# Optimization experiments

Hardware: AMD Instinct MI355X
Metric: run time of the kernel (lower is better)

The kernel has to match this reference:

```python
import jax, jax.numpy as jnp
import numpy as np

WIN = 9
WIN_SIZE = float(WIN ** 3)
LBD = 1.0
EPS = 1e-5


def _box_sum(x, win=WIN):
    """Separable sum over a win^3 window with zero padding == conv3d with all-ones kernel."""
    pad = win // 2
    for ax in (2, 3, 4):  # spatial axes of [N, C, H, W, D]
        wd = [1] * 5
        wd[ax] = win
        padc = [(0, 0)] * 5
        padc[ax] = (pad, pad)
        x = jax.lax.reduce_window(x, 0.0, jax.lax.add, tuple(wd), (1, 1, 1, 1, 1), padc)
    return x


def _warp3d(images, flows):
    """Trilinear warp. images [B,G,C,H,W,D], flows [B,G,3,H,W,D] (voxel displacements,
    channels ordered as (H, W, D) axes). Border-clamped sampling."""
    B, G, C, H, W, D = images.shape
    N = B * G
    img = images.reshape(N, C, H, W, D)
    flo = flows.reshape(N, 3, H, W, D)
    ft = flo.dtype
    gh = jnp.arange(H, dtype=ft).reshape(H, 1, 1)
    gw = jnp.arange(W, dtype=ft).reshape(1, W, 1)
    gd = jnp.arange(D, dtype=ft).reshape(1, 1, D)
    ch = jnp.clip(flo[:, 0] + gh, 0.0, H - 1.0)
    cw = jnp.clip(flo[:, 1] + gw, 0.0, W - 1.0)
    cd = jnp.clip(flo[:, 2] + gd, 0.0, D - 1.0)
    h0f = jnp.floor(ch); w0f = jnp.floor(cw); d0f = jnp.floor(cd)
    fh = ch - h0f; fw = cw - w0f; fd = cd - d0f
    h0 = h0f.astype(jnp.int32); w0 = w0f.astype(jnp.int32); d0 = d0f.astype(jnp.int32)
    h1 = jnp.minimum(h0 + 1, H - 1)
    w1 = jnp.minimum(w0 + 1, W - 1)
    d1 = jnp.minimum(d0 + 1, D - 1)
    flat = img.reshape(N, C, H * W * D)

    def gather(hi, wi, di):
        lin = ((hi * W + wi) * D + di).reshape(N, 1, H * W * D)
        return jnp.take_along_axis(flat, lin, axis=2).reshape(N, C, H, W, D)

    out = jnp.zeros_like(img)
    for hi, wh in ((h0, 1.0 - fh), (h1, fh)):
        for wi, ww in ((w0, 1.0 - fw), (w1, fw)):
            for di, wdw in ((d0, 1.0 - fd), (d1, fd)):
                w8 = (wh * ww * wdw)[:, None]  # [N,1,H,W,D]
                out = out + w8 * gather(hi, wi, di)
    return out.reshape(B, G, C, H, W, D)


def setup_inputs() -> dict:
    key = jax.random.key(0)
    k1, k2 = jax.random.split(key)
    images = jax.random.normal(k1, (1, 4, 1, 128, 128, 128), dtype=jnp.float32)
    warps = jax.random.normal(k2, (1, 4, 3, 128, 128, 128), dtype=jnp.float32)
    return {"images": images, "warps": warps}


def reference(images, warps):
    B, G, C, H, W, D = images.shape
    warped = _warp3d(images, warps).reshape(B * G, C, H, W, D)
    # groupwise template = mean over the B*G warped volumes, broadcast back
    template = jnp.broadcast_to(jnp.mean(warped, axis=0, keepdims=True), warped.shape)
    Ii, Ji = template, warped
    # 5 stat channels: I, J, I^2, J^2, IJ; groups=5 box-filter conv == per-channel box sum
    stats = jnp.concatenate([Ii, Ji, Ii * Ii, Ji * Ji, Ii * Ji], axis=1)
    sums = _box_sum(stats)
    I_sum, J_sum, I2_sum, J2_sum, IJ_sum = jnp.split(sums, 5, axis=1)
    cross = IJ_sum - J_sum / WIN_SIZE * I_sum
    I_var = I2_sum - I_sum / WIN_SIZE * I_sum
    J_var = J2_sum - J_sum / WIN_SIZE * J_sum
    cc = cross * cross / (I_var * J_var + EPS)
    lncc = -jnp.mean(cc)
    # Grad3d('l2') on warps [B,G,3,H,W,D]: dx over H (axis 3), dy over W (axis 4), dz over D (axis 5)
    dx = jnp.square(warps[:, :, :, 1:] - warps[:, :, :, :-1])
    dy = jnp.square(warps[:, :, :, :, 1:] - warps[:, :, :, :, :-1])
    dz = jnp.square(warps[..., 1:] - warps[..., :-1])
    g2 = (jnp.mean(dx) + jnp.mean(dy) + jnp.mean(dz)) / 3.0
    return lncc + LBD * g2
```

## Files before the change

### kernel.cpp

```cpp
#include <hip/hip_runtime.h>
#include <hip/hip_bf16.h>


#define NVOX (128*128*128)
#define NGRP 4
#define NCH 14

__global__ __launch_bounds__(256) void k_warp_stats_d(
    const float* __restrict__ img, const float* __restrict__ flo,
    float* __restrict__ S, double* __restrict__ pg2, int blk0)
{
    __shared__ float jt[NGRP][256];
    int t = threadIdx.x;
    int b = blk0 + ((blockIdx.x & 7) << 8) + (blockIdx.x >> 3);
    int v = b * 256 + t;
    int d = v & 127;
    int w = (v >> 7) & 127;
    int h = v >> 14;
    float g2s = 0.f;

#pragma unroll
    for (int g = 0; g < NGRP; ++g) {
        const float* f = flo + (size_t)g * 3 * NVOX;
        float fx = f[v], fy = f[NVOX + v], fz = f[2 * NVOX + v];
        if (h < 127) {
            float a = f[v + 16384] - fx;
            float bb = f[NVOX + v + 16384] - fy;
            float c = f[2 * NVOX + v + 16384] - fz;
            g2s += a * a + bb * bb + c * c;
        }
        if (w < 127) {
            float a = f[v + 128] - fx;
            float bb = f[NVOX + v + 128] - fy;
            float c = f[2 * NVOX + v + 128] - fz;
            g2s += a * a + bb * bb + c * c;
        }
        if (d < 127) {
            float a = f[v + 1] - fx;
            float bb = f[NVOX + v + 1] - fy;
            float c = f[2 * NVOX + v + 1] - fz;
            g2s += a * a + bb * bb + c * c;
        }
        float ch = fminf(fmaxf(fx + (float)h, 0.f), 127.f);
        float cw = fminf(fmaxf(fy + (float)w, 0.f), 127.f);
        float cd = fminf(fmaxf(fz + (float)d, 0.f), 127.f);
        float h0f = floorf(ch), w0f = floorf(cw), d0f = floorf(cd);
        int h0 = (int)h0f, w0 = (int)w0f, d0 = (int)d0f;
        float fh = ch - h0f, fw = cw - w0f, fd = cd - d0f;
        int h1 = min(h0 + 1, 127), w1 = min(w0 + 1, 127), d1 = min(d0 + 1, 127);
        const float* im = img + (size_t)g * NVOX;
        int b00 = (h0 * 128 + w0) * 128;
        int b01 = (h0 * 128 + w1) * 128;
        int b10 = (h1 * 128 + w0) * 128;
        int b11 = (h1 * 128 + w1) * 128;
        float v000 = im[b00 + d0], v001 = im[b00 + d1];
        float v010 = im[b01 + d0], v011 = im[b01 + d1];
        float v100 = im[b10 + d0], v101 = im[b10 + d1];
        float v110 = im[b11 + d0], v111 = im[b11 + d1];
        float c00 = v000 + fd * (v001 - v000);
        float c01 = v010 + fd * (v011 - v010);
        float c10 = v100 + fd * (v101 - v100);
        float c11 = v110 + fd * (v111 - v110);
        float c0 = c00 + fw * (c01 - c00);
        float c1 = c10 + fw * (c11 - c10);
        jt[g][t] = c0 + fh * (c1 - c0);
    }
    __syncthreads();

    float s[NCH];
#pragma unroll
    for (int c = 0; c < NCH; ++c) s[c] = 0.f;
    int lbase = t & 128;
#pragma unroll
    for (int k = -4; k <= 4; ++k) {
        int q = d + k;
        if ((unsigned)q < 128u) {
            int tq = lbase + q;
            float j0 = jt[0][tq], j1 = jt[1][tq], j2 = jt[2][tq], j3 = jt[3][tq];
            float tm = 0.25f * (j0 + j1 + j2 + j3);
            s[0] += tm;       s[1] += tm * tm;
            s[2] += j0;  s[3] += j0 * j0;  s[4]  += tm * j0;
            s[5] += j1;  s[6] += j1 * j1;  s[7]  += tm * j1;
            s[8] += j2;  s[9] += j2 * j2;  s[10] += tm * j2;
            s[11] += j3; s[12] += j3 * j3; s[13] += tm * j3;
        }
    }
#pragma unroll
    for (int c = 0; c < NCH; ++c) S[(size_t)c * NVOX + v] = s[c];

    double val = (double)g2s;
    for (int off = 32; off; off >>= 1) val += __shfl_down(val, off, 64);
    __shared__ double wsum[4];
    int lane = t & 63, wid = t >> 6;
    if (lane == 0) wsum[wid] = val;
    __syncthreads();
    if (t == 0) pg2[b] = wsum[0] + wsum[1] + wsum[2] + wsum[3];
}

__global__ __launch_bounds__(256) void k_sum_w(float* __restrict__ S)
{
    __shared__ float tile[128 * 68];
    int t = threadIdx.x;
    int bid = blockIdx.x;
    int half = bid & 1;
    int chh = bid >> 1;
    size_t base = (size_t)chh * 16384 + half * 64;
#pragma unroll
    for (int it = 0; it < 8; ++it) {
        int idx4 = it * 256 + t;
        int w = idx4 >> 4, dq = idx4 & 15;
        *(float4*)(tile + w * 68 + dq * 4) =
            *(const float4*)(S + base + (size_t)w * 128 + dq * 4);
    }
    __syncthreads();
    int dq = t & 15;
    int wq = t >> 4;
    int w0 = wq * 8;
    float4 s = make_float4(0.f, 0.f, 0.f, 0.f);
#pragma unroll
    for (int k = -4; k <= 4; ++k) {
        int q = w0 + k;
        if ((unsigned)q < 128u) {
            float4 tv = *(const float4*)(tile + q * 68 + dq * 4);
            s.x += tv.x; s.y += tv.y; s.z += tv.z; s.w += tv.w;
        }
    }
    *(float4*)(S + base + (size_t)w0 * 128 + dq * 4) = s;
#pragma unroll
    for (int wi = 1; wi < 8; ++wi) {
        int w = w0 + wi;
        int qa = w + 4;
        if (qa < 128) {
            float4 tv = *(const float4*)(tile + qa * 68 + dq * 4);
            s.x += tv.x; s.y += tv.y; s.z += tv.z; s.w += tv.w;
        }
        int qr = w - 5;
        if (qr >= 0) {
            float4 tv = *(const float4*)(tile + qr * 68 + dq * 4);
            s.x -= tv.x; s.y -= tv.y; s.z -= tv.z; s.w -= tv.w;
        }
        *(float4*)(S + base + (size_t)w * 128 + dq * 4) = s;
    }
}

__device__ __forceinline__ float cc4(float4 I, float4 I2, float4 J, float4 J2, float4 IJ)
{
    const float inv = 1.0f / 729.0f;
    float r = 0.f;
    {
        float cr = IJ.x - J.x * I.x * inv, iv = I2.x - I.x * I.x * inv, jv = J2.x - J.x * J.x * inv;
        r += cr * cr / (iv * jv + 1e-5f);
    }
    {
        float cr = IJ.y - J.y * I.y * inv, iv = I2.y - I.y * I.y * inv, jv = J2.y - J.y * J.y * inv;
        r += cr * cr / (iv * jv + 1e-5f);
    }
    {
        float cr = IJ.z - J.z * I.z * inv, iv = I2.z - I.z * I.z * inv, jv = J2.z - J.z * J.z * inv;
        r += cr * cr / (iv * jv + 1e-5f);
    }
    {
        float cr = IJ.w - J.w * I.w * inv, iv = I2.w - I.w * I.w * inv, jv = J2.w - J.w * J.w * inv;
        r += cr * cr / (iv * jv + 1e-5f);
    }
    return r;
}

#define LOADH(c, a0, a1)                                                       \
    do {                                                                       \
        const float* cp = S + (size_t)(c) * NVOX + cbase;                      \
        _Pragma("unroll")                                                      \
        for (int it = 0; it < 3; ++it) {                                       \
            int idx = it * 256 + t;                                            \
            if (idx < 640) {                           \
                int row = idx >> 4, dqu = idx & 15;                            \
                int rr = r0 + row;                                             \
                float4 vv = make_float4(0.f, 0.f, 0.f, 0.f);                   \
                if ((unsigned)rr < 128u)                                       \
                    vv = *(const float4*)(cp + (size_t)rr * 16384 + dqu * 4);  \
                int la = row * 65 + dqu * 4;                                   \
                tile[la] = vv.x; tile[la + 1] = vv.y;                          \
                tile[la + 2] = vv.z; tile[la + 3] = vv.w;                      \
            }                                                                  \
        }                                                                      \
        __syncthreads();                                                       \
        {                                                                      \
            int hl = hg * 2;                                                   \
            float4 sum = make_float4(0.f, 0.f, 0.f, 0.f);                      \
            _Pragma("unroll")                                                  \
            for (int k = 0; k < 9; ++k) {                                      \
                const float* tp = tile + (hl + k) * 65 + dq * 4;               \
                sum.x += tp[0]; sum.y += tp[1]; sum.z += tp[2]; sum.w += tp[3];\
            }                                                                  \
            a0 = sum;                                                          \
            const float* ta = tile + (hl + 9) * 65 + dq * 4;                   \
            const float* tr = tile + hl * 65 + dq * 4;                         \
            sum.x += ta[0] - tr[0]; sum.y += ta[1] - tr[1];                    \
            sum.z += ta[2] - tr[2]; sum.w += ta[3] - tr[3];                    \
            a1 = sum;                                                          \
        }                                                                      \
        __syncthreads();                                                       \
    } while (0)

__global__ __launch_bounds__(256) void k_sum_h_cc(const float* __restrict__ S,
                                                  double* __restrict__ pcc)
{
    __shared__ float tile[40 * 65];
    int t = threadIdx.x;
    int bid = blockIdx.x;
    int dh = bid & 1;
    int hq = (bid >> 1) & 3;
    int w = bid >> 3;
    int r0 = hq * 32 - 4;
    size_t cbase = (size_t)w * 128 + dh * 64;
    int dq = t & 15;
    int hg = t >> 4;

    float4 Ia0, Ia1, I2a0, I2a1, Ja0, Ja1, J2a0, J2a1, IJa0, IJa1;
    float lsum = 0.f;

    LOADH(0, Ia0, Ia1);
    LOADH(1, I2a0, I2a1);
    for (int g = 0; g < NGRP; ++g) {
        LOADH(2 + 3 * g, Ja0, Ja1);
        LOADH(3 + 3 * g, J2a0, J2a1);
        LOADH(4 + 3 * g, IJa0, IJa1);
        lsum += cc4(Ia0, I2a0, Ja0, J2a0, IJa0);
        lsum += cc4(Ia1, I2a1, Ja1, J2a1, IJa1);
    }

    double val = (double)lsum;
    for (int off = 32; off; off >>= 1) val += __shfl_down(val, off, 64);
    __shared__ double wsum[4];
    int lane = t & 63, wid = t >> 6;
    if (lane == 0) wsum[wid] = val;
    __syncthreads();
    if (t == 0) pcc[bid] = wsum[0] + wsum[1] + wsum[2] + wsum[3];
}

__global__ __launch_bounds__(256) void k_finalize(const double* __restrict__ pg2,
                                                  const double* __restrict__ pcc,
                                                  float* __restrict__ out)
{
    double s_cc = 0.0, s_g2 = 0.0;
    for (int i = threadIdx.x; i < 1024; i += 256) s_cc += pcc[i];
    for (int i = threadIdx.x; i < 8192; i += 256) s_g2 += pg2[i];
    for (int off = 32; off; off >>= 1) {
        s_cc += __shfl_down(s_cc, off, 64);
        s_g2 += __shfl_down(s_g2, off, 64);
    }
    __shared__ double a[4], b[4];
    int lane = threadIdx.x & 63, wid = threadIdx.x >> 6;
    if (lane == 0) { a[wid] = s_cc; b[wid] = s_g2; }
    __syncthreads();
    if (threadIdx.x == 0) {
        double cc_sum = a[0] + a[1] + a[2] + a[3];
        double g2_sum = b[0] + b[1] + b[2] + b[3];
        double lncc = -cc_sum / (4.0 * (double)NVOX);
        double g2 = g2_sum / (3.0 * 12.0 * 127.0 * 128.0 * 128.0);
        out[0] = (float)(lncc + g2);
    }
}

extern "C" void kernel_launch(void* const* d_in, const int* in_sizes, int n_in,
                              void* d_out, int out_size, void* d_ws, size_t ws_size,
                              hipStream_t stream)
{
    const float* img = (const float*)d_in[0];
    const float* flo = (const float*)d_in[1];
    float* out = (float*)d_out;

    const size_t S_BYTES = (size_t)NCH * NVOX * 4;
    float* S = (float*)d_ws;
    double* pg2 = (double*)((char*)d_ws + S_BYTES);
    double* pcc = pg2 + 8192;

    k_warp_stats_d<<<2048, 256, 0, stream>>>(img, flo, S, pg2, 0);
    k_warp_stats_d<<<2048, 256, 0, stream>>>(img, flo, S, pg2, 2048);
    k_warp_stats_d<<<2048, 256, 0, stream>>>(img, flo, S, pg2, 4096);
    k_warp_stats_d<<<2048, 256, 0, stream>>>(img, flo, S, pg2, 6144);
    k_sum_w<<<NCH * 128 * 2, 256, 0, stream>>>(S);
    k_sum_h_cc<<<1024, 256, 0, stream>>>(S, pcc);
    k_finalize<<<1, 256, 0, stream>>>(pg2, pcc, out);
}
```

Measured before the change: 351.5 us.

## Pack adjacent-depth image pairs to halve warp gathers; use nontemporal stores

Adds a pre-pass that packs each image voxel with its +1 depth neighbour into a float2 buffer. The trilinear warp can then fetch 4 paired loads instead of 8 scalar gathers. The four chunked warp-stats launches are merged into one launch with a new block swizzle. Stats stores and loads in all passes use nontemporal builtins, and the cc math is vectorised. The trade is an extra 32MB write and read for the packed buffer and a changed cache policy on the S traffic.

New measurement: 408.9 us. 16.3% more time.

```diff
diff --git a/kernel.cpp b/kernel.cpp
--- a/kernel.cpp
+++ b/kernel.cpp
@@ -6,13 +6,30 @@
 #define NGRP 4
 #define NCH 14
 
+typedef float f32x4 __attribute__((ext_vector_type(4)));
+typedef float f32x2 __attribute__((ext_vector_type(2)));
+
+__global__ __launch_bounds__(256) void k_pack2(const float* __restrict__ img,
+                                               f32x2* __restrict__ P2)
+{
+    int idx = blockIdx.x * 256 + threadIdx.x;
+    int v = idx & (NVOX - 1);
+    int g = idx >> 21;
+    int d = v & 127;
+    const float* im = img + (size_t)g * NVOX;
+    float a = im[v];
+    float b = (d < 127) ? im[v + 1] : a;
+    f32x2 pv; pv.x = a; pv.y = b;
+    __builtin_nontemporal_store(pv, &P2[idx]);
+}
+
 __global__ __launch_bounds__(256) void k_warp_stats_d(
-    const float* __restrict__ img, const float* __restrict__ flo,
-    float* __restrict__ S, double* __restrict__ pg2, int blk0)
+    const f32x2* __restrict__ P2, const float* __restrict__ flo,
+    float* __restrict__ S, double* __restrict__ pg2)
 {
     __shared__ float jt[NGRP][256];
     int t = threadIdx.x;
-    int b = blk0 + ((blockIdx.x & 7) << 8) + (blockIdx.x >> 3);
+    int b = ((blockIdx.x & 7) << 10) | (blockIdx.x >> 3);
     int v = b * 256 + t;
     int d = v & 127;
     int w = (v >> 7) & 127;
@@ -47,20 +64,16 @@
         float h0f = floorf(ch), w0f = floorf(cw), d0f = floorf(cd);
         int h0 = (int)h0f, w0 = (int)w0f, d0 = (int)d0f;
         float fh = ch - h0f, fw = cw - w0f, fd = cd - d0f;
-        int h1 = min(h0 + 1, 127), w1 = min(w0 + 1, 127), d1 = min(d0 + 1, 127);
-        const float* im = img + (size_t)g * NVOX;
-        int b00 = (h0 * 128 + w0) * 128;
-        int b01 = (h0 * 128 + w1) * 128;
-        int b10 = (h1 * 128 + w0) * 128;
-        int b11 = (h1 * 128 + w1) * 128;
-        float v000 = im[b00 + d0], v001 = im[b00 + d1];
-        float v010 = im[b01 + d0], v011 = im[b01 + d1];
-        float v100 = im[b10 + d0], v101 = im[b10 + d1];
-        float v110 = im[b11 + d0], v111 = im[b11 + d1];
-        float c00 = v000 + fd * (v001 - v000);
-        float c01 = v010 + fd * (v011 - v010);
-        float c10 = v100 + fd * (v101 - v100);
-        float c11 = v110 + fd * (v111 - v110);
+        int h1 = min(h0 + 1, 127), w1 = min(w0 + 1, 127);
+        const f32x2* P = P2 + (size_t)g * NVOX;
+        f32x2 q00 = P[h0 * 16384 + w0 * 128 + d0];
+        f32x2 q01 = P[h0 * 16384 + w1 * 128 + d0];
+        f32x2 q10 = P[h1 * 16384 + w0 * 128 + d0];
+        f32x2 q11 = P[h1 * 16384 + w1 * 128 + d0];
+        float c00 = q00.x + fd * (q00.y - q00.x);
+        float c01 = q01.x + fd * (q01.y - q01.x);
+        float c10 = q10.x + fd * (q10.y - q10.x);
+        float c11 = q11.x + fd * (q11.y - q11.x);
         float c0 = c00 + fw * (c01 - c00);
         float c1 = c10 + fw * (c11 - c10);
         jt[g][t] = c0 + fh * (c1 - c0);
@@ -86,7 +99,8 @@
         }
     }
 #pragma unroll
-    for (int c = 0; c < NCH; ++c) S[(size_t)c * NVOX + v] = s[c];
+    for (int c = 0; c < NCH; ++c)
+        __builtin_nontemporal_store(s[c], &S[(size_t)c * NVOX + v]);
 
     double val = (double)g2s;
     for (int off = 32; off; off >>= 1) val += __shfl_down(val, off, 64);
@@ -109,61 +123,43 @@
     for (int it = 0; it < 8; ++it) {
         int idx4 = it * 256 + t;
         int w = idx4 >> 4, dq = idx4 & 15;
-        *(float4*)(tile + w * 68 + dq * 4) =
-            *(const float4*)(S + base + (size_t)w * 128 + dq * 4);
+        f32x4 vv = __builtin_nontemporal_load(
+            (const f32x4*)(S + base + (size_t)w * 128 + dq * 4));
+        *(f32x4*)(tile + w * 68 + dq * 4) = vv;
     }
     __syncthreads();
     int dq = t & 15;
     int wq = t >> 4;
     int w0 = wq * 8;
-    float4 s = make_float4(0.f, 0.f, 0.f, 0.f);
+    f32x4 s = {0.f, 0.f, 0.f, 0.f};
 #pragma unroll
     for (int k = -4; k <= 4; ++k) {
         int q = w0 + k;
-        if ((unsigned)q < 128u) {
-            float4 tv = *(const float4*)(tile + q * 68 + dq * 4);
-            s.x += tv.x; s.y += tv.y; s.z += tv.z; s.w += tv.w;
-        }
-    }
-    *(float4*)(S + base + (size_t)w0 * 128 + dq * 4) = s;
+        if ((unsigned)q < 128u)
+            s += *(const f32x4*)(tile + q * 68 + dq * 4);
+    }
+    __builtin_nontemporal_store(s, (f32x4*)(S + base + (size_t)w0 * 128 + dq * 4));
 #pragma unroll
     for (int wi = 1; wi < 8; ++wi) {
         int w = w0 + wi;
         int qa = w + 4;
-        if (qa < 128) {
-            float4 tv = *(const float4*)(tile + qa * 68 + dq * 4);
-            s.x += tv.x; s.y += tv.y; s.z += tv.z; s.w += tv.w;
-        }
+        if (qa < 128)
+            s += *(const f32x4*)(tile + qa * 68 + dq * 4);
         int qr = w - 5;
-        if (qr >= 0) {
-            float4 tv = *(const float4*)(tile + qr * 68 + dq * 4);
-            s.x -= tv.x; s.y -= tv.y; s.z -= tv.z; s.w -= tv.w;
-        }
-        *(float4*)(S + base + (size_t)w * 128 + dq * 4) = s;
-    }
-}
-
-__device__ __forceinline__ float cc4(float4 I, float4 I2, float4 J, float4 J2, float4 IJ)
+        if (qr >= 0)
+            s -= *(const f32x4*)(tile + qr * 68 + dq * 4);
+        __builtin_nontemporal_store(s, (f32x4*)(S + base + (size_t)w * 128 + dq * 4));
+    }
+}
+
+__device__ __forceinline__ float cc4(f32x4 I, f32x4 I2, f32x4 J, f32x4 J2, f32x4 IJ)
 {
     const float inv = 1.0f / 729.0f;
-    float r = 0.f;
-    {
-        float cr = IJ.x - J.x * I.x * inv, iv = I2.x - I.x * I.x * inv, jv = J2.x - J.x * J.x * inv;
-        r += cr * cr / (iv * jv + 1e-5f);
-    }
-    {
-        float cr = IJ.y - J.y * I.y * inv, iv = I2.y - I.y * I.y * inv, jv = J2.y - J.y * J.y * inv;
-        r += cr * cr / (iv * jv + 1e-5f);
-    }
-    {
-        float cr = IJ.z - J.z * I.z * inv, iv = I2.z - I.z * I.z * inv, jv = J2.z - J.z * J.z * inv;
-        r += cr * cr / (iv * jv + 1e-5f);
-    }
-    {
-        float cr = IJ.w - J.w * I.w * inv, iv = I2.w - I.w * I.w * inv, jv = J2.w - J.w * J.w * inv;
-        r += cr * cr / (iv * jv + 1e-5f);
-    }
-    return r;
+    f32x4 cr = IJ - J * I * inv;
+    f32x4 iv = I2 - I * I * inv;
+    f32x4 jv = J2 - J * J * inv;
+    f32x4 cc = cr * cr / (iv * jv + 1e-5f);
+    return cc.x + cc.y + cc.z + cc.w;
 }
 
 #define LOADH(c, a0, a1)                                                       \
@@ -175,9 +171,10 @@
             if (idx < 640) {                           \
                 int row = idx >> 4, dqu = idx & 15;                            \
                 int rr = r0 + row;                                             \
-                float4 vv = make_float4(0.f, 0.f, 0.f, 0.f);                   \
+                f32x4 vv = {0.f, 0.f, 0.f, 0.f};                               \
                 if ((unsigned)rr < 128u)                                       \
-                    vv = *(const float4*)(cp + (size_t)rr * 16384 + dqu * 4);  \
+                    vv = __builtin_nontemporal_load(                           \
+                        (const f32x4*)(cp + (size_t)rr * 16384 + dqu * 4));    \
                 int la = row * 65 + dqu * 4;                                   \
                 tile[la] = vv.x; tile[la + 1] = vv.y;                          \
                 tile[la + 2] = vv.z; tile[la + 3] = vv.w;                      \
@@ -186,7 +183,7 @@
         __syncthreads();                                                       \
         {                                                                      \
             int hl = hg * 2;                                                   \
-            float4 sum = make_float4(0.f, 0.f, 0.f, 0.f);                      \
+            f32x4 sum = {0.f, 0.f, 0.f, 0.f};                                  \
             _Pragma("unroll")                                                  \
             for (int k = 0; k < 9; ++k) {                                      \
                 const float* tp = tile + (hl + k) * 65 + dq * 4;               \
@@ -216,7 +213,7 @@
     int dq = t & 15;
     int hg = t >> 4;
 
-    float4 Ia0, Ia1, I2a0, I2a1, Ja0, Ja1, J2a0, J2a1, IJa0, IJa1;
+    f32x4 Ia0, Ia1, I2a0, I2a1, Ja0, Ja1, J2a0, J2a1, IJa0, IJa1;
     float lsum = 0.f;
 
     LOADH(0, Ia0, Ia1);
@@ -270,15 +267,15 @@
     const float* flo = (const float*)d_in[1];
     float* out = (float*)d_out;
 
-    const size_t S_BYTES = (size_t)NCH * NVOX * 4;
+    const size_t S_BYTES  = (size_t)NCH * NVOX * 4;
+    const size_t P2_BYTES = (size_t)NGRP * NVOX * 8;
     float* S = (float*)d_ws;
-    double* pg2 = (double*)((char*)d_ws + S_BYTES);
+    f32x2* P2 = (f32x2*)((char*)d_ws + S_BYTES);
+    double* pg2 = (double*)((char*)d_ws + S_BYTES + P2_BYTES);
     double* pcc = pg2 + 8192;
 
-    k_warp_stats_d<<<2048, 256, 0, stream>>>(img, flo, S, pg2, 0);
-    k_warp_stats_d<<<2048, 256, 0, stream>>>(img, flo, S, pg2, 2048);
-    k_warp_stats_d<<<2048, 256, 0, stream>>>(img, flo, S, pg2, 4096);
-    k_warp_stats_d<<<2048, 256, 0, stream>>>(img, flo, S, pg2, 6144);
+    k_pack2<<<(NGRP * NVOX) / 256, 256, 0, stream>>>(img, P2);
+    k_warp_stats_d<<<NVOX / 256, 256, 0, stream>>>(P2, flo, S, pg2);
     k_sum_w<<<NCH * 128 * 2, 256, 0, stream>>>(S);
     k_sum_h_cc<<<1024, 256, 0, stream>>>(S, pcc);
     k_finalize<<<1, 256, 0, stream>>>(pg2, pcc, out);
```
